# Kernel tuning notes

Hardware: AMD Instinct MI355X
Metric: run time of the kernel (lower is better)

Reference implementation:

```python
import jax, jax.numpy as jnp
import numpy as np

B, T, D = 2, 2048, 1024
H = 16
HD = D // H  # 64


def setup_inputs() -> dict:
    key = jax.random.key(0)
    ks = jax.random.split(key, 5)
    s = 0.02
    return {
        "x": jax.random.normal(ks[0], (B, T, D), dtype=jnp.float32),
        "Wqkv": jax.random.normal(ks[1], (D, 3 * D), dtype=jnp.float32) * s,
        "bqkv": jnp.zeros((3 * D,), dtype=jnp.float32),
        "Wproj": jax.random.normal(ks[2], (D, D), dtype=jnp.float32) * s,
        "bproj": jnp.zeros((D,), dtype=jnp.float32),
    }


def _rope(q, k, seq_len, head_dim):
    half = head_dim // 2
    idx = jnp.arange(half, dtype=jnp.float32)
    pos = jnp.arange(seq_len, dtype=jnp.float32)[:, None]  # [T,1]
    rates = jnp.power(10000.0, -2.0 * idx / head_dim)       # [half]
    theta = pos * rates                                      # [T,half]
    cos = jnp.cos(theta)
    sin = jnp.sin(theta)

    def apply(x):  # x: [B,H,T,HD]
        x1 = x[..., :half]
        x2 = x[..., half:half * 2]
        return jnp.concatenate([x1 * cos - x2 * sin, x1 * sin + x2 * cos], axis=-1)

    return apply(q), apply(k)


def reference(x, Wqkv, bqkv, Wproj, bproj):
    b, t, c = x.shape
    qkv = x @ Wqkv + bqkv                       # [B,T,3D]
    q, k, v = jnp.split(qkv, 3, axis=-1)
    q = q.reshape(b, t, H, HD).transpose(0, 2, 1, 3)  # [B,H,T,HD]
    k = k.reshape(b, t, H, HD).transpose(0, 2, 1, 3)
    v = v.reshape(b, t, H, HD).transpose(0, 2, 1, 3)
    q, k = _rope(q, k, t, HD)
    scale = HD ** -0.5
    scores = jnp.einsum('bhqd,bhkd->bhqk', q, k) * scale
    causal = jnp.tril(jnp.ones((t, t), dtype=bool))
    scores = jnp.where(causal, scores, jnp.float32(-jnp.inf))
    attn = jax.nn.softmax(scores, axis=-1)
    y = jnp.einsum('bhqk,bhkd->bhqd', attn, v)  # [B,H,T,HD]
    y = y.transpose(0, 2, 1, 3).reshape(b, t, c)
    return y @ Wproj + bproj
```

## Files before the change

kernel.cpp:

```cpp
#include <hip/hip_runtime.h>
#include <hip/hip_bf16.h>
#include <cstdint>

#define BB 2
#define TT 2048
#define DD 1024
#define HH 16
#define HD 64
#define BT (BB*TT)
#define QKV_N (3*DD)

typedef __attribute__((ext_vector_type(8))) short  short8;
typedef __attribute__((ext_vector_type(4))) float  f32x4;
typedef __attribute__((ext_vector_type(16))) float f32x16;

static __device__ __forceinline__ ushort f2bf(float f) {
    union { float f; uint32_t u; } v; v.f = f;
    uint32_t u = v.u;
    return (ushort)((u + 0x7FFFu + ((u >> 16) & 1u)) >> 16);
}

typedef const __attribute__((address_space(1))) uint32_t* gp1_t;
typedef __attribute__((address_space(3))) uint32_t* lp3_t;
static __device__ __forceinline__ void gload_lds16(const void* g, void* l) {
    __builtin_amdgcn_global_load_lds((gp1_t)g, (lp3_t)l, 16, 0, 0);
}

static __device__ __forceinline__ uint32_t cvtpk_bf16(float a, float b) {
    uint32_t r;
    asm volatile("v_cvt_pk_bf16_f32 %0, %1, %2" : "=v"(r) : "v"(a), "v"(b));
    return r;
}
static __device__ __forceinline__ void pl32swap(uint32_t& a, uint32_t& b) {
    asm volatile("v_permlane32_swap_b32 %0, %1" : "+v"(a), "+v"(b));
}
static __device__ __forceinline__ float fexp2(float x) {
    float r; asm("v_exp_f32 %0, %1" : "=v"(r) : "v"(x)); return r;
}

static __device__ __forceinline__ f32x16 mfma32(short8 a, short8 b, f32x16 c) {
    return __builtin_amdgcn_mfma_f32_32x32x16_bf16(a, b, c, 0, 0, 0);
}

#define QSCALE 0.18033688011112042f

__global__ __launch_bounds__(256) void f32_to_bf16(
    const float* __restrict__ in, ushort* __restrict__ out, int n8)
{
    const int i = blockIdx.x * 256 + threadIdx.x;
    if (i >= n8) return;
    float4 v0 = *(const float4*)(in + (size_t)i * 8);
    float4 v1 = *(const float4*)(in + (size_t)i * 8 + 4);
    ushort o[8] = {f2bf(v0.x), f2bf(v0.y), f2bf(v0.z), f2bf(v0.w),
                   f2bf(v1.x), f2bf(v1.y), f2bf(v1.z), f2bf(v1.w)};
    *(short8*)(out + (size_t)i * 8) = *(const short8*)o;
}

__global__ __launch_bounds__(256) void rope_tab(float2* __restrict__ ctab)
{
    const int idx = blockIdx.x * 256 + threadIdx.x;
    const int i = idx & 31;
    const int t = idx >> 5;
    const float rate = powf(10000.0f, -(float)i * (1.0f / 32.0f));
    const float th = (float)t * rate;
    ctab[idx] = make_float2(cosf(th), sinf(th));
}

__global__ __launch_bounds__(256) void transpose_w_bf16(
    const float* __restrict__ W, ushort* __restrict__ Wt, int K, int N)
{
    __shared__ ushort Ws[64][72];
    const int n0 = blockIdx.x * 64;
    const int k0 = blockIdx.y * 64;
    const int tid = threadIdx.x;

    #pragma unroll
    for (int it = 0; it < 4; ++it) {
        const int r  = it * 16 + (tid >> 4);
        const int c4 = (tid & 15) * 4;
        float4 v = *(const float4*)&W[(size_t)(k0 + r) * N + n0 + c4];
        Ws[c4 + 0][r] = f2bf(v.x);
        Ws[c4 + 1][r] = f2bf(v.y);
        Ws[c4 + 2][r] = f2bf(v.z);
        Ws[c4 + 3][r] = f2bf(v.w);
    }
    __syncthreads();
    #pragma unroll
    for (int it = 0; it < 2; ++it) {
        const int rn = it * 32 + (tid >> 3);
        const int c8 = (tid & 7) * 8;
        *(short8*)&Wt[(size_t)(n0 + rn) * K + k0 + c8] = *(const short8*)&Ws[rn][c8];
    }
}

__global__ __launch_bounds__(256) void gemm_proj(
    const ushort* __restrict__ A, const ushort* __restrict__ Bt,
    const float* __restrict__ bias, float* __restrict__ C,
    int M, int N, int K)
{
    __shared__ __align__(16) ushort As[128 * 64];
    __shared__ __align__(16) ushort Bs[128 * 64];

    const int nbx = N >> 7;
    const int nwg = (M >> 7) * nbx;
    const int cpx = nwg >> 3;
    const int bid = blockIdx.x;
    const int lb  = (bid & 7) * cpx + (bid >> 3);
    const int n0 = (lb % nbx) * 128;
    const int m0 = (lb / nbx) * 128;

    const int tid = threadIdx.x;
    const int w  = tid >> 6, l = tid & 63;
    const int lr = l & 15,  lg = l >> 4;
    const int wm = w >> 1,  wn = w & 1;

    f32x4 acc[4][4] = {};

    for (int k0 = 0; k0 < K; k0 += 64) {
        #pragma unroll
        for (int i = 0; i < 4; ++i) {
            const int f = i * 256 + w * 64 + l;
            const int r = f >> 3, c = f & 7;
            gload_lds16(A + (size_t)(m0 + r) * K + k0 + ((c ^ (r & 7)) << 3),
                        &As[(i * 256 + w * 64) * 8]);
        }
        #pragma unroll
        for (int i = 0; i < 4; ++i) {
            const int f = i * 256 + w * 64 + l;
            const int r = f >> 3, c = f & 7;
            gload_lds16(Bt + (size_t)(n0 + r) * K + k0 + ((c ^ (r & 7)) << 3),
                        &Bs[(i * 256 + w * 64) * 8]);
        }
        __syncthreads();

        #pragma unroll
        for (int kk = 0; kk < 2; ++kk) {
            short8 a[4], b[4];
            #pragma unroll
            for (int mi = 0; mi < 4; ++mi) {
                const int row = wm * 64 + mi * 16 + lr;
                const int c   = kk * 4 + lg;
                a[mi] = *(const short8*)&As[row * 64 + ((c ^ (row & 7)) << 3)];
            }
            #pragma unroll
            for (int ni = 0; ni < 4; ++ni) {
                const int row = wn * 64 + ni * 16 + lr;
                const int c   = kk * 4 + lg;
                b[ni] = *(const short8*)&Bs[row * 64 + ((c ^ (row & 7)) << 3)];
            }
            #pragma unroll
            for (int mi = 0; mi < 4; ++mi)
                #pragma unroll
                for (int ni = 0; ni < 4; ++ni)
                    acc[mi][ni] = __builtin_amdgcn_mfma_f32_16x16x32_bf16(
                        a[mi], b[ni], acc[mi][ni], 0, 0, 0);
        }
        __syncthreads();
    }

    #pragma unroll
    for (int mi = 0; mi < 4; ++mi) {
        #pragma unroll
        for (int ni = 0; ni < 4; ++ni) {
            const int n = n0 + wn * 64 + ni * 16 + lr;
            const float bv = bias[n];
            #pragma unroll
            for (int j = 0; j < 4; ++j) {
                const int m = m0 + wm * 64 + mi * 16 + lg * 4 + j;
                C[(size_t)m * N + n] = acc[mi][ni][j] + bv;
            }
        }
    }
}

__global__ __launch_bounds__(256) void gemm_qkv_fused(
    const ushort* __restrict__ A,
    const ushort* __restrict__ Bt,
    const float*  __restrict__ bias,
    const float2* __restrict__ ctab,
    ushort* __restrict__ Qb, ushort* __restrict__ Kswz, ushort* __restrict__ Vswz)
{
    __shared__ __align__(16) ushort As[128 * 64];
    __shared__ __align__(16) ushort Bs[128 * 64];

    const int nbx = QKV_N >> 7;
    const int cpx = ((BT >> 7) * nbx) >> 3;
    const int bid = blockIdx.x;
    const int lb  = (bid & 7) * cpx + (bid >> 3);
    const int n0 = (lb % nbx) * 128;
    const int m0 = (lb / nbx) * 128;

    const int tid = threadIdx.x;
    const int w  = tid >> 6, l = tid & 63;
    const int lr = l & 15,  lg = l >> 4;
    const int wm = w >> 1,  wn = w & 1;

    f32x4 acc[4][4] = {};

    for (int k0 = 0; k0 < DD; k0 += 64) {
        #pragma unroll
        for (int i = 0; i < 4; ++i) {
            const int f = i * 256 + w * 64 + l;
            const int r = f >> 3, c = f & 7;
            gload_lds16(A + (size_t)(m0 + r) * DD + k0 + ((c ^ (r & 7)) << 3),
                        &As[(i * 256 + w * 64) * 8]);
        }
        #pragma unroll
        for (int i = 0; i < 4; ++i) {
            const int f = i * 256 + w * 64 + l;
            const int r = f >> 3, c = f & 7;
            gload_lds16(Bt + (size_t)(n0 + r) * DD + k0 + ((c ^ (r & 7)) << 3),
                        &Bs[(i * 256 + w * 64) * 8]);
        }
        __syncthreads();

        #pragma unroll
        for (int kk = 0; kk < 2; ++kk) {
            short8 a[4], b[4];
            #pragma unroll
            for (int mi = 0; mi < 4; ++mi) {
                const int row = wm * 64 + mi * 16 + lr;
                const int c   = kk * 4 + lg;
                a[mi] = *(const short8*)&As[row * 64 + ((c ^ (row & 7)) << 3)];
            }
            #pragma unroll
            for (int ni = 0; ni < 4; ++ni) {
                const int row = wn * 64 + ni * 16 + lr;
                const int c   = kk * 4 + lg;
                b[ni] = *(const short8*)&Bs[row * 64 + ((c ^ (row & 7)) << 3)];
            }
            #pragma unroll
            for (int mi = 0; mi < 4; ++mi)
                #pragma unroll
                for (int ni = 0; ni < 4; ++ni)
                    acc[mi][ni] = __builtin_amdgcn_mfma_f32_16x16x32_bf16(
                        a[mi], b[ni], acc[mi][ni], 0, 0, 0);
        }
        __syncthreads();
    }

    const int g64  = n0 + wn * 64;
    const int part = g64 >> 10;
    const int h    = (g64 & 1023) >> 6;

    float bv[4];
    #pragma unroll
    for (int ni = 0; ni < 4; ++ni) bv[ni] = bias[g64 + ni * 16 + lr];

    #pragma unroll
    for (int mi = 0; mi < 4; ++mi) {
        #pragma unroll
        for (int j = 0; j < 4; ++j) {
            const int m  = m0 + wm * 64 + mi * 16 + lg * 4 + j;
            const int bb = m >> 11;
            const int t  = m & (TT - 1);
            const int bh = bb * HH + h;
            const float v0 = acc[mi][0][j] + bv[0];
            const float v1 = acc[mi][1][j] + bv[1];
            const float v2 = acc[mi][2][j] + bv[2];
            const float v3 = acc[mi][3][j] + bv[3];

            if (part == 2) {
                ushort* vb = Vswz + (size_t)bh * (TT * HD) + (t >> 6) * 4096
                           + ((t & 63) >> 4) * 512 + ((t >> 3) & 1) * 256
                           + (t & 7) + lr * 8;
                vb[0]    = f2bf(v0);
                vb[128]  = f2bf(v1);
                vb[2048] = f2bf(v2);
                vb[2176] = f2bf(v3);
            } else {
                const float2 cs0 = ctab[t * 32 + lr];
                const float2 cs1 = ctab[t * 32 + 16 + lr];
                float r0 = v0 * cs0.x - v2 * cs0.y;
                float r2 = v0 * cs0.y + v2 * cs0.x;
                float r1 = v1 * cs1.x - v3 * cs1.y;
                float r3 = v1 * cs1.y + v3 * cs1.x;
                if (part == 0) {
                    r0 *= QSCALE; r1 *= QSCALE; r2 *= QSCALE; r3 *= QSCALE;
                    ushort* qb = Qb + (size_t)bh * (TT * HD) + t * HD + lr;
                    qb[0]  = f2bf(r0);
                    qb[16] = f2bf(r1);
                    qb[32] = f2bf(r2);
                    qb[48] = f2bf(r3);
                } else {
                    ushort* kb = Kswz + (size_t)bh * (TT * HD) + (t >> 6) * 4096
                               + ((t >> 5) & 1) * 2048 + (t & 31) * 8
                               + ((lr >> 3) & 1) * 256 + (lr & 7);
                    kb[0]    = f2bf(r0);
                    kb[512]  = f2bf(r1);
                    kb[1024] = f2bf(r2);
                    kb[1536] = f2bf(r3);
                }
            }
        }
    }
}

__global__ __launch_bounds__(256) void attn_splitk(
    const ushort* __restrict__ Qb, const ushort* __restrict__ Kswz,
    const ushort* __restrict__ Vswz, ushort* __restrict__ y)
{
    __shared__ float Lacc[4][32][64];
    __shared__ float Ll[4][32];

    const int bid = blockIdx.x;
    const int bh  = bid & 31;
    const int qt  = 63 - (bid >> 5);
    const int b   = bh >> 4;
    const int h   = bh & 15;
    const int tid = threadIdx.x;
    const int w   = tid >> 6;
    const int l   = tid & 63;
    const int lq  = l & 31;
    const int hi  = l >> 5;

    const int wq0 = qt * 32;
    const int qg  = wq0 + lq;

    const ushort* Kbh = Kswz + (size_t)bh * TT * HD;
    const ushort* Vbh = Vswz + (size_t)bh * TT * HD;

    short8 qf[4];
    {
        const ushort* qrow = Qb + ((size_t)bh * TT + qg) * HD + hi * 8;
        #pragma unroll
        for (int dc = 0; dc < 4; ++dc)
            qf[dc] = *(const short8*)(qrow + dc * 16);
    }

    f32x16 acc0 = {}, acc1 = {};
    float lsum = 0.0f;

    const int nt = (wq0 >> 6) + 1;

    for (int t = w; t < nt; t += 4) {
        const int k0 = t * 64;
        const ushort* kb = Kbh + (size_t)t * 4096 + l * 8;
        const ushort* vb = Vbh + (size_t)t * 4096 + l * 8;

        short8 kf0[4], kf1[4], vf0[4], vf1[4];
        #pragma unroll
        for (int dc = 0; dc < 4; ++dc) {
            kf0[dc] = *(const short8*)(kb + dc * 512);
            kf1[dc] = *(const short8*)(kb + (4 + dc) * 512);
            vf0[dc] = *(const short8*)(vb + dc * 512);
            vf1[dc] = *(const short8*)(vb + (4 + dc) * 512);
        }

        f32x16 st0 = {}, st1 = {};
        __builtin_amdgcn_s_setprio(1);
        #pragma unroll
        for (int dc = 0; dc < 4; ++dc) {
            st0 = mfma32(kf0[dc], qf[dc], st0);
            st1 = mfma32(kf1[dc], qf[dc], st1);
        }
        __builtin_amdgcn_s_setprio(0);

        if (t == nt - 1) {
            #pragma unroll
            for (int r = 0; r < 16; ++r) {
                const int kk = k0 + (r & 3) + 8 * (r >> 2) + 4 * hi;
                if (kk > qg)      st0[r] = -1e30f;
                if (kk + 32 > qg) st1[r] = -1e30f;
            }
        }

        #pragma unroll
        for (int r = 0; r < 16; ++r) {
            st0[r] = fexp2(st0[r]);
            st1[r] = fexp2(st1[r]);
        }
        float rs;
        {
            float s16[16];
            #pragma unroll
            for (int i = 0; i < 16; ++i) s16[i] = st0[i] + st1[i];
            float s8[8];
            #pragma unroll
            for (int i = 0; i < 8; ++i) s8[i] = s16[i] + s16[i + 8];
            rs = ((s8[0] + s8[4]) + (s8[1] + s8[5]))
               + ((s8[2] + s8[6]) + (s8[3] + s8[7]));
        }
        rs += __shfl_xor(rs, 32);
        lsum += rs;

        short8 pfr[4];
        #pragma unroll
        for (int sub = 0; sub < 2; ++sub) {
            const f32x16& ps = sub ? st1 : st0;
            uint32_t A0 = cvtpk_bf16(ps[0],  ps[1]);
            uint32_t A1 = cvtpk_bf16(ps[2],  ps[3]);
            uint32_t B0 = cvtpk_bf16(ps[4],  ps[5]);
            uint32_t B1 = cvtpk_bf16(ps[6],  ps[7]);
            uint32_t C0 = cvtpk_bf16(ps[8],  ps[9]);
            uint32_t C1 = cvtpk_bf16(ps[10], ps[11]);
            uint32_t D0 = cvtpk_bf16(ps[12], ps[13]);
            uint32_t D1 = cvtpk_bf16(ps[14], ps[15]);
            pl32swap(A0, B0); pl32swap(A1, B1);
            pl32swap(C0, D0); pl32swap(C1, D1);
            union { uint32_t u[4]; short8 s; } f0, f1;
            f0.u[0] = A0; f0.u[1] = A1; f0.u[2] = B0; f0.u[3] = B1;
            f1.u[0] = C0; f1.u[1] = C1; f1.u[2] = D0; f1.u[3] = D1;
            pfr[sub * 2]     = f0.s;
            pfr[sub * 2 + 1] = f1.s;
        }

        __builtin_amdgcn_s_setprio(1);
        #pragma unroll
        for (int kc = 0; kc < 4; ++kc) {
            acc0 = mfma32(pfr[kc], vf0[kc], acc0);
            acc1 = mfma32(pfr[kc], vf1[kc], acc1);
        }
        __builtin_amdgcn_s_setprio(0);
    }

    #pragma unroll
    for (int r = 0; r < 16; ++r) {
        Lacc[w][r][l]      = acc0[r];
        Lacc[w][r + 16][l] = acc1[r];
    }
    if (hi == 0) Ll[w][lq] = lsum;
    __syncthreads();

    const int r0 = w * 8;
    #pragma unroll
    for (int i = 0; i < 8; ++i) {
        const int r   = r0 + i;
        const int rr  = r & 15;
        const int row = (rr & 3) + 8 * (rr >> 2) + 4 * hi;
        const float L = Ll[0][row] + Ll[1][row] + Ll[2][row] + Ll[3][row];
        float o = Lacc[0][r][l] + Lacc[1][r][l] + Lacc[2][r][l] + Lacc[3][r][l];
        o *= (1.0f / L);
        const int d = (r < 16) ? lq : (32 + lq);
        y[((size_t)b * TT + wq0 + row) * DD + h * HD + d] = f2bf(o);
    }
}

extern "C" void kernel_launch(void* const* d_in, const int* in_sizes, int n_in,
                              void* d_out, int out_size, void* d_ws, size_t ws_size,
                              hipStream_t stream)
{
    const float* x     = (const float*)d_in[0];
    const float* Wqkv  = (const float*)d_in[1];
    const float* bqkv  = (const float*)d_in[2];
    const float* Wproj = (const float*)d_in[3];
    const float* bproj = (const float*)d_in[4];
    float* out = (float*)d_out;

    ushort* yb     = (ushort*)d_ws;
    ushort* Qb     = yb     + (size_t)BT * DD;
    ushort* Kswz   = Qb     + (size_t)BB * HH * TT * HD;
    ushort* Vswz   = Kswz   + (size_t)BB * HH * TT * HD;
    ushort* xb     = Vswz   + (size_t)BB * HH * TT * HD;
    ushort* Wqkvt  = xb     + (size_t)BT * DD;
    ushort* Wprojt = Wqkvt  + (size_t)QKV_N * DD;
    float2* ctab   = (float2*)(Wprojt + (size_t)DD * DD);

    f32_to_bf16<<<(BT * DD / 8 + 255) / 256, 256, 0, stream>>>(x, xb, BT * DD / 8);
    rope_tab<<<TT * 32 / 256, 256, 0, stream>>>(ctab);
    {
        dim3 g1(QKV_N / 64, DD / 64);
        transpose_w_bf16<<<g1, 256, 0, stream>>>(Wqkv, Wqkvt, DD, QKV_N);
        dim3 g2(DD / 64, DD / 64);
        transpose_w_bf16<<<g2, 256, 0, stream>>>(Wproj, Wprojt, DD, DD);
    }
    {
        gemm_qkv_fused<<<(BT / 128) * (QKV_N / 128), 256, 0, stream>>>(
            xb, Wqkvt, bqkv, ctab, Qb, Kswz, Vswz);
    }
    {
        attn_splitk<<<2048, 256, 0, stream>>>(Qb, Kswz, Vswz, yb);
    }
    {
        gemm_proj<<<(BT / 128) * (DD / 128), 256, 0, stream>>>(
            yb, Wprojt, bproj, out, BT, DD, DD);
    }
}
```

Measured before the change: 114.7 us.

## Process two 32-row query tiles per block to share K/V fragment loads

The attention kernel now handles a 64-row query block as two 32-row halves in each workgroup, so every K/V tile loaded from global memory feeds both halves' MFMAs. The grid is halved, and the second half's QK^T MFMAs are interleaved with the first half's PV MFMAs to overlap matrix work with the softmax arithmetic. In exchange it uses more registers for the extra accumulators and Q fragments, which may lower occupancy. The epilogue adds an extra LDS reduction pass with another barrier.

```diff
diff --git a/kernel.cpp b/kernel.cpp
--- a/kernel.cpp
+++ b/kernel.cpp
@@ -296,7 +296,7 @@
     }
 }
 
-__global__ __launch_bounds__(256) void attn_splitk(
+__global__ __launch_bounds__(256) void attn_pair(
     const ushort* __restrict__ Qb, const ushort* __restrict__ Kswz,
     const ushort* __restrict__ Vswz, ushort* __restrict__ y)
 {
@@ -305,7 +305,7 @@
 
     const int bid = blockIdx.x;
     const int bh  = bid & 31;
-    const int qt  = 63 - (bid >> 5);
+    const int j   = 31 - (bid >> 5);
     const int b   = bh >> 4;
     const int h   = bh & 15;
     const int tid = threadIdx.x;
@@ -314,80 +314,89 @@
     const int lq  = l & 31;
     const int hi  = l >> 5;
 
-    const int wq0 = qt * 32;
-    const int qg  = wq0 + lq;
+    const int wq0A = j * 64;
+    const int wq0B = wq0A + 32;
+    const int qgA  = wq0A + lq;
 
     const ushort* Kbh = Kswz + (size_t)bh * TT * HD;
     const ushort* Vbh = Vswz + (size_t)bh * TT * HD;
 
-    short8 qf[4];
+    short8 qfA[4], qfB[4];
     {
-        const ushort* qrow = Qb + ((size_t)bh * TT + qg) * HD + hi * 8;
-        #pragma unroll
-        for (int dc = 0; dc < 4; ++dc)
-            qf[dc] = *(const short8*)(qrow + dc * 16);
-    }
-
-    f32x16 acc0 = {}, acc1 = {};
-    float lsum = 0.0f;
-
-    const int nt = (wq0 >> 6) + 1;
+        const ushort* qa = Qb + ((size_t)bh * TT + qgA) * HD + hi * 8;
+        #pragma unroll
+        for (int dc = 0; dc < 4; ++dc) {
+            qfA[dc] = *(const short8*)(qa + dc * 16);
+            qfB[dc] = *(const short8*)(qa + 32 * HD + dc * 16);
+        }
+    }
+
+    f32x16 accA0 = {}, accA1 = {};
+    f32x16 accB0 = {}, accB1 = {};
+    float lsumA = 0.0f, lsumB = 0.0f;
+
+    const int nt = j + 1;
 
     for (int t = w; t < nt; t += 4) {
         const int k0 = t * 64;
         const ushort* kb = Kbh + (size_t)t * 4096 + l * 8;
         const ushort* vb = Vbh + (size_t)t * 4096 + l * 8;
-
-        short8 kf0[4], kf1[4], vf0[4], vf1[4];
+        const bool diag = (t == nt - 1);
+
+        short8 kf0[4], kf1[4];
         #pragma unroll
         for (int dc = 0; dc < 4; ++dc) {
             kf0[dc] = *(const short8*)(kb + dc * 512);
             kf1[dc] = *(const short8*)(kb + (4 + dc) * 512);
+        }
+
+        f32x16 sA0 = {}, sA1 = {};
+        __builtin_amdgcn_s_setprio(1);
+        #pragma unroll
+        for (int dc = 0; dc < 4; ++dc) {
+            sA0 = mfma32(kf0[dc], qfA[dc], sA0);
+            sA1 = mfma32(kf1[dc], qfA[dc], sA1);
+        }
+        __builtin_amdgcn_s_setprio(0);
+
+        short8 vf0[4], vf1[4];
+        #pragma unroll
+        for (int dc = 0; dc < 4; ++dc) {
             vf0[dc] = *(const short8*)(vb + dc * 512);
             vf1[dc] = *(const short8*)(vb + (4 + dc) * 512);
         }
 
-        f32x16 st0 = {}, st1 = {};
-        __builtin_amdgcn_s_setprio(1);
-        #pragma unroll
-        for (int dc = 0; dc < 4; ++dc) {
-            st0 = mfma32(kf0[dc], qf[dc], st0);
-            st1 = mfma32(kf1[dc], qf[dc], st1);
-        }
-        __builtin_amdgcn_s_setprio(0);
-
-        if (t == nt - 1) {
+        if (diag) {
             #pragma unroll
             for (int r = 0; r < 16; ++r) {
-                const int kk = k0 + (r & 3) + 8 * (r >> 2) + 4 * hi;
-                if (kk > qg)      st0[r] = -1e30f;
-                if (kk + 32 > qg) st1[r] = -1e30f;
+                const int keyloc = (r & 3) + 8 * (r >> 2) + 4 * hi;
+                if (keyloc > lq) sA0[r] = -1e30f;
+                sA1[r] = -1e30f;
             }
         }
 
         #pragma unroll
         for (int r = 0; r < 16; ++r) {
-            st0[r] = fexp2(st0[r]);
-            st1[r] = fexp2(st1[r]);
-        }
-        float rs;
+            sA0[r] = fexp2(sA0[r]);
+            sA1[r] = fexp2(sA1[r]);
+        }
         {
             float s16[16];
             #pragma unroll
-            for (int i = 0; i < 16; ++i) s16[i] = st0[i] + st1[i];
+            for (int i = 0; i < 16; ++i) s16[i] = sA0[i] + sA1[i];
             float s8[8];
             #pragma unroll
             for (int i = 0; i < 8; ++i) s8[i] = s16[i] + s16[i + 8];
-            rs = ((s8[0] + s8[4]) + (s8[1] + s8[5]))
-               + ((s8[2] + s8[6]) + (s8[3] + s8[7]));
-        }
-        rs += __shfl_xor(rs, 32);
-        lsum += rs;
-
-        short8 pfr[4];
+            float rs = ((s8[0] + s8[4]) + (s8[1] + s8[5]))
+                     + ((s8[2] + s8[6]) + (s8[3] + s8[7]));
+            rs += __shfl_xor(rs, 32);
+            lsumA += rs;
+        }
+
+        short8 pfrA[4];
         #pragma unroll
         for (int sub = 0; sub < 2; ++sub) {
-            const f32x16& ps = sub ? st1 : st0;
+            const f32x16& ps = sub ? sA1 : sA0;
             uint32_t A0 = cvtpk_bf16(ps[0],  ps[1]);
             uint32_t A1 = cvtpk_bf16(ps[2],  ps[3]);
             uint32_t B0 = cvtpk_bf16(ps[4],  ps[5]);
@@ -401,25 +410,86 @@
             union { uint32_t u[4]; short8 s; } f0, f1;
             f0.u[0] = A0; f0.u[1] = A1; f0.u[2] = B0; f0.u[3] = B1;
             f1.u[0] = C0; f1.u[1] = C1; f1.u[2] = D0; f1.u[3] = D1;
-            pfr[sub * 2]     = f0.s;
-            pfr[sub * 2 + 1] = f1.s;
-        }
-
+            pfrA[sub * 2]     = f0.s;
+            pfrA[sub * 2 + 1] = f1.s;
+        }
+
+        f32x16 sB0 = {}, sB1 = {};
         __builtin_amdgcn_s_setprio(1);
         #pragma unroll
+        for (int dc = 0; dc < 4; ++dc) {
+            sB0 = mfma32(kf0[dc], qfB[dc], sB0);
+            sB1 = mfma32(kf1[dc], qfB[dc], sB1);
+        }
+        #pragma unroll
         for (int kc = 0; kc < 4; ++kc) {
-            acc0 = mfma32(pfr[kc], vf0[kc], acc0);
-            acc1 = mfma32(pfr[kc], vf1[kc], acc1);
+            accA0 = mfma32(pfrA[kc], vf0[kc], accA0);
+            accA1 = mfma32(pfrA[kc], vf1[kc], accA1);
         }
         __builtin_amdgcn_s_setprio(0);
+
+        if (diag) {
+            #pragma unroll
+            for (int r = 0; r < 16; ++r) {
+                const int keyloc = (r & 3) + 8 * (r >> 2) + 4 * hi;
+                if (keyloc > lq) sB1[r] = -1e30f;
+            }
+        }
+
+        #pragma unroll
+        for (int r = 0; r < 16; ++r) {
+            sB0[r] = fexp2(sB0[r]);
+            sB1[r] = fexp2(sB1[r]);
+        }
+        {
+            float s16[16];
+            #pragma unroll
+            for (int i = 0; i < 16; ++i) s16[i] = sB0[i] + sB1[i];
+            float s8[8];
+            #pragma unroll
+            for (int i = 0; i < 8; ++i) s8[i] = s16[i] + s16[i + 8];
+            float rs = ((s8[0] + s8[4]) + (s8[1] + s8[5]))
+                     + ((s8[2] + s8[6]) + (s8[3] + s8[7]));
+            rs += __shfl_xor(rs, 32);
+            lsumB += rs;
+        }
+
+        short8 pfrB[4];
+        #pragma unroll
+        for (int sub = 0; sub < 2; ++sub) {
+            const f32x16& ps = sub ? sB1 : sB0;
+            uint32_t A0 = cvtpk_bf16(ps[0],  ps[1]);
+            uint32_t A1 = cvtpk_bf16(ps[2],  ps[3]);
+            uint32_t B0 = cvtpk_bf16(ps[4],  ps[5]);
+            uint32_t B1 = cvtpk_bf16(ps[6],  ps[7]);
+            uint32_t C0 = cvtpk_bf16(ps[8],  ps[9]);
+            uint32_t C1 = cvtpk_bf16(ps[10], ps[11]);
+            uint32_t D0 = cvtpk_bf16(ps[12], ps[13]);
+            uint32_t D1 = cvtpk_bf16(ps[14], ps[15]);
+            pl32swap(A0, B0); pl32swap(A1, B1);
+            pl32swap(C0, D0); pl32swap(C1, D1);
+            union { uint32_t u[4]; short8 s; } f0, f1;
+            f0.u[0] = A0; f0.u[1] = A1; f0.u[2] = B0; f0.u[3] = B1;
+            f1.u[0] = C0; f1.u[1] = C1; f1.u[2] = D0; f1.u[3] = D1;
+            pfrB[sub * 2]     = f0.s;
+            pfrB[sub * 2 + 1] = f1.s;
+        }
+
+        __builtin_amdgcn_s_setprio(1);
+        #pragma unroll
+        for (int kc = 0; kc < 4; ++kc) {
+            accB0 = mfma32(pfrB[kc], vf0[kc], accB0);
+            accB1 = mfma32(pfrB[kc], vf1[kc], accB1);
+        }
+        __builtin_amdgcn_s_setprio(0);
     }
 
     #pragma unroll
     for (int r = 0; r < 16; ++r) {
-        Lacc[w][r][l]      = acc0[r];
-        Lacc[w][r + 16][l] = acc1[r];
-    }
-    if (hi == 0) Ll[w][lq] = lsum;
+        Lacc[w][r][l]      = accA0[r];
+        Lacc[w][r + 16][l] = accA1[r];
+    }
+    if (hi == 0) Ll[w][lq] = lsumA;
     __syncthreads();
 
     const int r0 = w * 8;
@@ -432,7 +502,28 @@
         float o = Lacc[0][r][l] + Lacc[1][r][l] + Lacc[2][r][l] + Lacc[3][r][l];
         o *= (1.0f / L);
         const int d = (r < 16) ? lq : (32 + lq);
-        y[((size_t)b * TT + wq0 + row) * DD + h * HD + d] = f2bf(o);
+        y[((size_t)b * TT + wq0A + row) * DD + h * HD + d] = f2bf(o);
+    }
+    __syncthreads();
+
+    #pragma unroll
+    for (int r = 0; r < 16; ++r) {
+        Lacc[w][r][l]      = accB0[r];
+        Lacc[w][r + 16][l] = accB1[r];
+    }
+    if (hi == 0) Ll[w][lq] = lsumB;
+    __syncthreads();
+
+    #pragma unroll
+    for (int i = 0; i < 8; ++i) {
+        const int r   = r0 + i;
+        const int rr  = r & 15;
+        const int row = (rr & 3) + 8 * (rr >> 2) + 4 * hi;
+        const float L = Ll[0][row] + Ll[1][row] + Ll[2][row] + Ll[3][row];
+        float o = Lacc[0][r][l] + Lacc[1][r][l] + Lacc[2][r][l] + Lacc[3][r][l];
+        o *= (1.0f / L);
+        const int d = (r < 16) ? lq : (32 + lq);
+        y[((size_t)b * TT + wq0B + row) * DD + h * HD + d] = f2bf(o);
     }
 }
 
@@ -469,7 +560,7 @@
             xb, Wqkvt, bqkv, ctab, Qb, Kswz, Vswz);
     }
     {
-        attn_splitk<<<2048, 256, 0, stream>>>(Qb, Kswz, Vswz, yb);
+        attn_pair<<<1024, 256, 0, stream>>>(Qb, Kswz, Vswz, yb);
     }
     {
         gemm_proj<<<(BT / 128) * (DD / 128), 256, 0, stream>>>(
```

After: 119.7 us. 1.04x slower.

## Share K/V tiles in LDS across four query-tile waves with double buffering

Applied to the files above, without the earlier changes.

Replaces the split-K attention kernel, where each block's four waves split the key range of one 32-row query tile and reduce through LDS, with a kernel in which each wave owns its own query tile. The block's 128 consecutive query rows share K/V tiles staged into double-buffered LDS via async global-to-LDS loads. This cuts redundant global K/V reads and removes the cross-wave reduction, but the grid shrinks from 2048 to 512 blocks. It also adds a block-wide barrier per key tile and causes causal imbalance, since waves with fewer tiles sit idle at the barriers.

```diff
diff --git a/kernel.cpp b/kernel.cpp
--- a/kernel.cpp
+++ b/kernel.cpp
@@ -296,16 +296,16 @@
     }
 }
 
-__global__ __launch_bounds__(256) void attn_splitk(
+__global__ __launch_bounds__(256) void attn_lds(
     const ushort* __restrict__ Qb, const ushort* __restrict__ Kswz,
     const ushort* __restrict__ Vswz, ushort* __restrict__ y)
 {
-    __shared__ float Lacc[4][32][64];
-    __shared__ float Ll[4][32];
+    __shared__ __align__(16) ushort Ks[2][4096];
+    __shared__ __align__(16) ushort Vs[2][4096];
 
     const int bid = blockIdx.x;
     const int bh  = bid & 31;
-    const int qt  = 63 - (bid >> 5);
+    const int m   = 15 - (bid >> 5);
     const int b   = bh >> 4;
     const int h   = bh & 15;
     const int tid = threadIdx.x;
@@ -314,8 +314,11 @@
     const int lq  = l & 31;
     const int hi  = l >> 5;
 
-    const int wq0 = qt * 32;
-    const int qg  = wq0 + lq;
+    const int qt    = m * 4 + w;
+    const int wq0   = qt * 32;
+    const int qg    = wq0 + lq;
+    const int nt    = (wq0 >> 6) + 1;
+    const int ntmax = 2 * m + 2;
 
     const ushort* Kbh = Kswz + (size_t)bh * TT * HD;
     const ushort* Vbh = Vswz + (size_t)bh * TT * HD;
@@ -331,108 +334,117 @@
     f32x16 acc0 = {}, acc1 = {};
     float lsum = 0.0f;
 
-    const int nt = (wq0 >> 6) + 1;
-
-    for (int t = w; t < nt; t += 4) {
-        const int k0 = t * 64;
-        const ushort* kb = Kbh + (size_t)t * 4096 + l * 8;
-        const ushort* vb = Vbh + (size_t)t * 4096 + l * 8;
-
-        short8 kf0[4], kf1[4], vf0[4], vf1[4];
-        #pragma unroll
-        for (int dc = 0; dc < 4; ++dc) {
-            kf0[dc] = *(const short8*)(kb + dc * 512);
-            kf1[dc] = *(const short8*)(kb + (4 + dc) * 512);
-            vf0[dc] = *(const short8*)(vb + dc * 512);
-            vf1[dc] = *(const short8*)(vb + (4 + dc) * 512);
-        }
-
-        f32x16 st0 = {}, st1 = {};
-        __builtin_amdgcn_s_setprio(1);
-        #pragma unroll
-        for (int dc = 0; dc < 4; ++dc) {
-            st0 = mfma32(kf0[dc], qf[dc], st0);
-            st1 = mfma32(kf1[dc], qf[dc], st1);
-        }
-        __builtin_amdgcn_s_setprio(0);
-
-        if (t == nt - 1) {
+    #define STAGE_T(t, buf)                                                    \
+        do {                                                                   \
+            _Pragma("unroll")                                                  \
+            for (int i_ = 0; i_ < 2; ++i_) {                                   \
+                const int base_ = i_ * 256 + w * 64;                           \
+                gload_lds16(Kbh + (size_t)(t) * 4096 + (size_t)(base_ + l) * 8,\
+                            &Ks[buf][base_ * 8]);                              \
+                gload_lds16(Vbh + (size_t)(t) * 4096 + (size_t)(base_ + l) * 8,\
+                            &Vs[buf][base_ * 8]);                              \
+            }                                                                  \
+        } while (0)
+
+    STAGE_T(0, 0);
+    __syncthreads();
+
+    for (int t = 0; t < ntmax; ++t) {
+        const int cur = t & 1;
+
+        if (t + 1 < ntmax) STAGE_T(t + 1, cur ^ 1);
+
+        if (t < nt) {
+            const int k0 = t * 64;
+
+            short8 kf0[4], kf1[4], vf0[4], vf1[4];
+            #pragma unroll
+            for (int dc = 0; dc < 4; ++dc) {
+                kf0[dc] = *(const short8*)&Ks[cur][dc * 512 + l * 8];
+                kf1[dc] = *(const short8*)&Ks[cur][(4 + dc) * 512 + l * 8];
+                vf0[dc] = *(const short8*)&Vs[cur][dc * 512 + l * 8];
+                vf1[dc] = *(const short8*)&Vs[cur][(4 + dc) * 512 + l * 8];
+            }
+
+            f32x16 st0 = {}, st1 = {};
+            __builtin_amdgcn_s_setprio(1);
+            #pragma unroll
+            for (int dc = 0; dc < 4; ++dc) {
+                st0 = mfma32(kf0[dc], qf[dc], st0);
+                st1 = mfma32(kf1[dc], qf[dc], st1);
+            }
+            __builtin_amdgcn_s_setprio(0);
+
+            if (t == nt - 1) {
+                #pragma unroll
+                for (int r = 0; r < 16; ++r) {
+                    const int kk = k0 + (r & 3) + 8 * (r >> 2) + 4 * hi;
+                    if (kk > qg)      st0[r] = -1e30f;
+                    if (kk + 32 > qg) st1[r] = -1e30f;
+                }
+            }
+
             #pragma unroll
             for (int r = 0; r < 16; ++r) {
-                const int kk = k0 + (r & 3) + 8 * (r >> 2) + 4 * hi;
-                if (kk > qg)      st0[r] = -1e30f;
-                if (kk + 32 > qg) st1[r] = -1e30f;
-            }
-        }
-
-        #pragma unroll
-        for (int r = 0; r < 16; ++r) {
-            st0[r] = fexp2(st0[r]);
-            st1[r] = fexp2(st1[r]);
-        }
-        float rs;
-        {
-            float s16[16];
-            #pragma unroll
-            for (int i = 0; i < 16; ++i) s16[i] = st0[i] + st1[i];
-            float s8[8];
-            #pragma unroll
-            for (int i = 0; i < 8; ++i) s8[i] = s16[i] + s16[i + 8];
-            rs = ((s8[0] + s8[4]) + (s8[1] + s8[5]))
-               + ((s8[2] + s8[6]) + (s8[3] + s8[7]));
-        }
-        rs += __shfl_xor(rs, 32);
-        lsum += rs;
-
-        short8 pfr[4];
-        #pragma unroll
-        for (int sub = 0; sub < 2; ++sub) {
-            const f32x16& ps = sub ? st1 : st0;
-            uint32_t A0 = cvtpk_bf16(ps[0],  ps[1]);
-            uint32_t A1 = cvtpk_bf16(ps[2],  ps[3]);
-            uint32_t B0 = cvtpk_bf16(ps[4],  ps[5]);
-            uint32_t B1 = cvtpk_bf16(ps[6],  ps[7]);
-            uint32_t C0 = cvtpk_bf16(ps[8],  ps[9]);
-            uint32_t C1 = cvtpk_bf16(ps[10], ps[11]);
-            uint32_t D0 = cvtpk_bf16(ps[12], ps[13]);
-            uint32_t D1 = cvtpk_bf16(ps[14], ps[15]);
-            pl32swap(A0, B0); pl32swap(A1, B1);
-            pl32swap(C0, D0); pl32swap(C1, D1);
-            union { uint32_t u[4]; short8 s; } f0, f1;
-            f0.u[0] = A0; f0.u[1] = A1; f0.u[2] = B0; f0.u[3] = B1;
-            f1.u[0] = C0; f1.u[1] = C1; f1.u[2] = D0; f1.u[3] = D1;
-            pfr[sub * 2]     = f0.s;
-            pfr[sub * 2 + 1] = f1.s;
-        }
-
-        __builtin_amdgcn_s_setprio(1);
-        #pragma unroll
-        for (int kc = 0; kc < 4; ++kc) {
-            acc0 = mfma32(pfr[kc], vf0[kc], acc0);
-            acc1 = mfma32(pfr[kc], vf1[kc], acc1);
-        }
-        __builtin_amdgcn_s_setprio(0);
-    }
-
+                st0[r] = fexp2(st0[r]);
+                st1[r] = fexp2(st1[r]);
+            }
+            float rs;
+            {
+                float s16[16];
+                #pragma unroll
+                for (int i = 0; i < 16; ++i) s16[i] = st0[i] + st1[i];
+                float s8[8];
+                #pragma unroll
+                for (int i = 0; i < 8; ++i) s8[i] = s16[i] + s16[i + 8];
+                rs = ((s8[0] + s8[4]) + (s8[1] + s8[5]))
+                   + ((s8[2] + s8[6]) + (s8[3] + s8[7]));
+            }
+            rs += __shfl_xor(rs, 32);
+            lsum += rs;
+
+            short8 pfr[4];
+            #pragma unroll
+            for (int sub = 0; sub < 2; ++sub) {
+                const f32x16& ps = sub ? st1 : st0;
+                uint32_t A0 = cvtpk_bf16(ps[0],  ps[1]);
+                uint32_t A1 = cvtpk_bf16(ps[2],  ps[3]);
+                uint32_t B0 = cvtpk_bf16(ps[4],  ps[5]);
+                uint32_t B1 = cvtpk_bf16(ps[6],  ps[7]);
+                uint32_t C0 = cvtpk_bf16(ps[8],  ps[9]);
+                uint32_t C1 = cvtpk_bf16(ps[10], ps[11]);
+                uint32_t D0 = cvtpk_bf16(ps[12], ps[13]);
+                uint32_t D1 = cvtpk_bf16(ps[14], ps[15]);
+                pl32swap(A0, B0); pl32swap(A1, B1);
+                pl32swap(C0, D0); pl32swap(C1, D1);
+                union { uint32_t u[4]; short8 s; } f0, f1;
+                f0.u[0] = A0; f0.u[1] = A1; f0.u[2] = B0; f0.u[3] = B1;
+                f1.u[0] = C0; f1.u[1] = C1; f1.u[2] = D0; f1.u[3] = D1;
+                pfr[sub * 2]     = f0.s;
+                pfr[sub * 2 + 1] = f1.s;
+            }
+
+            __builtin_amdgcn_s_setprio(1);
+            #pragma unroll
+            for (int kc = 0; kc < 4; ++kc) {
+                acc0 = mfma32(pfr[kc], vf0[kc], acc0);
+                acc1 = mfma32(pfr[kc], vf1[kc], acc1);
+            }
+            __builtin_amdgcn_s_setprio(0);
+        }
+
+        __syncthreads();
+    }
+    #undef STAGE_T
+
+    const float inv = 1.0f / lsum;
     #pragma unroll
     for (int r = 0; r < 16; ++r) {
-        Lacc[w][r][l]      = acc0[r];
-        Lacc[w][r + 16][l] = acc1[r];
-    }
-    if (hi == 0) Ll[w][lq] = lsum;
-    __syncthreads();
-
-    const int r0 = w * 8;
-    #pragma unroll
-    for (int i = 0; i < 8; ++i) {
-        const int r   = r0 + i;
-        const int rr  = r & 15;
-        const int row = (rr & 3) + 8 * (rr >> 2) + 4 * hi;
-        const float L = Ll[0][row] + Ll[1][row] + Ll[2][row] + Ll[3][row];
-        float o = Lacc[0][r][l] + Lacc[1][r][l] + Lacc[2][r][l] + Lacc[3][r][l];
-        o *= (1.0f / L);
-        const int d = (r < 16) ? lq : (32 + lq);
-        y[((size_t)b * TT + wq0 + row) * DD + h * HD + d] = f2bf(o);
+        const int row = (r & 3) + 8 * (r >> 2) + 4 * hi;
+        const float ir = __shfl(inv, row);
+        ushort* yo = y + ((size_t)b * TT + wq0 + row) * DD + h * HD;
+        yo[lq]      = f2bf(acc0[r] * ir);
+        yo[32 + lq] = f2bf(acc1[r] * ir);
     }
 }
 
@@ -469,7 +481,7 @@
             xb, Wqkvt, bqkv, ctab, Qb, Kswz, Vswz);
     }
     {
-        attn_splitk<<<2048, 256, 0, stream>>>(Qb, Kswz, Vswz, yb);
+        attn_lds<<<512, 256, 0, stream>>>(Qb, Kswz, Vswz, yb);
     }
     {
         gemm_proj<<<(BT / 128) * (DD / 128), 256, 0, stream>>>(
```

Result: slower. 124.9 us (+8.9%).
